# Kernel optimization log

Hardware: AMD Instinct MI355X
Metric: run time of the kernel (lower is better)

The kernel has to match this reference:

```python
import jax, jax.numpy as jnp
import numpy as np

L, H, N = 4096, 256, 64  # seq_len, hidden_size, hippo_n
EPS = 1e-5


def setup_inputs() -> dict:
    key = jax.random.key(0)
    ks = jax.random.split(key, 8)
    x = jax.random.normal(ks[0], (L, H), jnp.float32)
    # S4D-Lin style initialization for the diagonal SSM (H independent SSMs of state size N)
    Lambda_re = -0.5 * jnp.ones((H, N), jnp.float32)
    Lambda_im = jnp.tile(jnp.pi * jnp.arange(N, dtype=jnp.float32), (H, 1))
    B_re = jnp.ones((H, N), jnp.float32)
    B_im = jnp.zeros((H, N), jnp.float32)
    C_re = jax.random.normal(ks[1], (H, N), jnp.float32) * (0.5 ** 0.5)
    C_im = jax.random.normal(ks[2], (H, N), jnp.float32) * (0.5 ** 0.5)
    D = jax.random.normal(ks[3], (H,), jnp.float32)
    log_step = jax.random.uniform(ks[4], (H,), jnp.float32,
                                  minval=jnp.log(0.001), maxval=jnp.log(0.1))
    ln_w = jnp.ones((H,), jnp.float32)
    ln_b = jnp.zeros((H,), jnp.float32)
    sc = 1.0 / jnp.sqrt(jnp.float32(H))
    W1 = jax.random.normal(ks[5], (H, H), jnp.float32) * sc
    b1 = jnp.zeros((H,), jnp.float32)
    W2 = jax.random.normal(ks[6], (H, H), jnp.float32) * sc
    b2 = jnp.zeros((H,), jnp.float32)
    return {"x": x, "Lambda_re": Lambda_re, "Lambda_im": Lambda_im,
            "B_re": B_re, "B_im": B_im, "C_re": C_re, "C_im": C_im,
            "D": D, "log_step": log_step, "ln_w": ln_w, "ln_b": ln_b,
            "W1": W1, "b1": b1, "W2": W2, "b2": b2}


def reference(x, Lambda_re, Lambda_im, B_re, B_im, C_re, C_im, D, log_step,
              ln_w, ln_b, W1, b1, W2, b2):
    skip = x
    # per-token LayerNorm over the H feature axis (eqx.nn.LayerNorm, eps=1e-5)
    mu = jnp.mean(x, axis=-1, keepdims=True)
    var = jnp.mean(jnp.square(x - mu), axis=-1, keepdims=True)
    xn = (x - mu) / jnp.sqrt(var + EPS) * ln_w + ln_b  # [L, H]

    # ZOH discretization of the diagonal SSM (the cell.ssm(L) step)
    Lam = Lambda_re + 1j * Lambda_im                     # [H, N] complex64
    dt = jnp.exp(log_step)[:, None]                      # [H, 1]
    Ab = jnp.exp(Lam * dt)                               # [H, N]
    Bb = (Ab - 1.0) / Lam * (B_re + 1j * B_im)           # [H, N]
    C = C_re + 1j * C_im                                 # [H, N]

    def step(s, u):  # s: [H, N] complex state, u: [H] input at one time step
        s = Ab * s + Bb * u[:, None]
        y = 2.0 * jnp.einsum('hn,hn->h', C, s).real + D * u
        return s, y

    s0 = jnp.zeros((H, N), jnp.complex64)
    hidden, ys = jax.lax.scan(step, s0, xn)              # ys: [L, H]

    g = jax.nn.gelu(ys)
    out = (g @ W1.T + b1) * jax.nn.sigmoid(g @ W2.T + b2)  # GLU epilogue
    return (hidden, skip + out)
```

## Files before the change

### kernel.cpp

```cpp
#include <hip/hip_runtime.h>
#include <hip/hip_bf16.h>

#define LSEQ 4096
#define HDIM 256
#define NS   64
#define PC   32
#define MC   128

typedef __attribute__((ext_vector_type(8))) short short8;
typedef __attribute__((ext_vector_type(4))) float floatx4;

__device__ __forceinline__ short b16(float x) {
    __hip_bfloat16 h = __float2bfloat16(x);
    return *(reinterpret_cast<short*>(&h));
}
__device__ __forceinline__ float bf2f(unsigned short u) {
    unsigned int v = ((unsigned int)u) << 16;
    return __uint_as_float(v);
}
__device__ __forceinline__ unsigned int pk2(float a, float b) {
    return (unsigned int)(unsigned short)b16(a) | ((unsigned int)(unsigned short)b16(b) << 16);
}
__device__ __forceinline__ void cmul(float& xr, float& xi, float yr, float yi) {
    float r = xr * yr - xi * yi;
    float i = xr * yi + xi * yr;
    xr = r; xi = i;
}

__global__ __launch_bounds__(256) void k_pre(const float* __restrict__ x,
                                             const float* __restrict__ lnw,
                                             const float* __restrict__ lnb,
                                             const float* __restrict__ W1,
                                             const float* __restrict__ W2,
                                             float* __restrict__ xnT,
                                             unsigned short* __restrict__ w1b,
                                             unsigned short* __restrict__ w2b) {
    int t = threadIdx.x;
    if (blockIdx.x >= 256) {
        int g = (blockIdx.x - 256) * 256 + t;
        float4 a = ((const float4*)W1)[g];
        float4 c = ((const float4*)W2)[g];
        ushort4 o1, o2;
        o1.x = (unsigned short)b16(a.x); o1.y = (unsigned short)b16(a.y);
        o1.z = (unsigned short)b16(a.z); o1.w = (unsigned short)b16(a.w);
        o2.x = (unsigned short)b16(c.x); o2.y = (unsigned short)b16(c.y);
        o2.z = (unsigned short)b16(c.z); o2.w = (unsigned short)b16(c.w);
        ((ushort4*)w1b)[g] = o1;
        ((ushort4*)w2b)[g] = o2;
        return;
    }
    __shared__ float tile[16][257];
    __shared__ float smu[16], srs[16];
    int l0 = blockIdx.x * 16;
#pragma unroll
    for (int i = 0; i < 16; ++i)
        tile[i][t] = x[(size_t)(l0 + i) * HDIM + t];
    __syncthreads();
    int wv = t >> 6, lane = t & 63;
#pragma unroll
    for (int k = 0; k < 4; ++k) {
        int i = wv * 4 + k;
        float s = 0.f, s2 = 0.f;
#pragma unroll
        for (int q = 0; q < 4; ++q) {
            float v = tile[i][lane + 64 * q];
            s += v; s2 += v * v;
        }
#pragma unroll
        for (int o = 32; o; o >>= 1) {
            s  += __shfl_xor(s, o);
            s2 += __shfl_xor(s2, o);
        }
        if (lane == 0) {
            float m = s * (1.0f / HDIM);
            smu[i] = m;
            srs[i] = rsqrtf(s2 * (1.0f / HDIM) - m * m + 1e-5f);
        }
    }
    __syncthreads();
    float wh = lnw[t], bh = lnb[t];
    float o[16];
#pragma unroll
    for (int i = 0; i < 16; ++i)
        o[i] = (tile[i][t] - smu[i]) * srs[i] * wh + bh;
    float4* dst = (float4*)(xnT + (size_t)t * LSEQ + l0);
#pragma unroll
    for (int k = 0; k < 4; ++k)
        dst[k] = make_float4(o[4 * k], o[4 * k + 1], o[4 * k + 2], o[4 * k + 3]);
}

__device__ __forceinline__ void ssm_consts(const float* Lre, const float* Lim,
                                           const float* Bre, const float* Bim,
                                           float dt, int idx,
                                           float& are, float& aim, float& bre, float& bim) {
    float lre = Lre[idx], lim = Lim[idx];
    float er = expf(lre * dt);
    float sa, ca;
    sincosf(lim * dt, &sa, &ca);
    are = er * ca; aim = er * sa;
    float inv = 1.0f / (lre * lre + lim * lim);
    float nre = are - 1.0f, nim = aim;
    float tre = (nre * lre + nim * lim) * inv;
    float tim = (nim * lre - nre * lim) * inv;
    float br = Bre[idx], bi = Bim[idx];
    bre = tre * br - tim * bi;
    bim = tre * bi + tim * br;
}

__global__ __launch_bounds__(512) void k_scan(const float* __restrict__ xnT,
                                              const float* __restrict__ Lre,
                                              const float* __restrict__ Lim,
                                              const float* __restrict__ Bre,
                                              const float* __restrict__ Bim,
                                              const float* __restrict__ Cre,
                                              const float* __restrict__ Cim,
                                              const float* __restrict__ Dv,
                                              const float* __restrict__ lstep,
                                              __hip_bfloat16* __restrict__ gb,
                                              float* __restrict__ hid,
                                              int interleaved) {
    __shared__ __align__(16) unsigned char ldsb[60672];
    short* ubf = (short*)(ldsb);
    short* Xm  = (short*)(ldsb + 8704);
    float* Ff  = (float*)(ldsb + 43520);
    short* S0s = (short*)(ldsb + 43520);
    float* Kt  = (float*)(ldsb + 60160);

    int h = blockIdx.x >> 1, half = blockIdx.x & 1;
    int tid = threadIdx.x;
    int wv = __builtin_amdgcn_readfirstlane(tid) >> 6;
    int lane = tid & 63;
    int l15 = lane & 15, q = lane >> 4;
    const float* uh = xnT + (size_t)h * LSEQ;

    float dt = expf(lstep[h]);
    float Dh = Dv[h];

    float are, aim, bre, bim;
    ssm_consts(Lre, Lim, Bre, Bim, dt, h * NS + lane, are, aim, bre, bim);
    float cre = Cre[h * NS + lane], cim = Cim[h * NS + lane];

    float A2r = are, A2i = aim;   cmul(A2r, A2i, are, aim);
    float A4r = A2r, A4i = A2i;   cmul(A4r, A4i, A2r, A2i);
    float A8r = A4r, A8i = A4i;   cmul(A8r, A8i, A4r, A4i);
    float A16r = A8r, A16i = A8i;  cmul(A16r, A16i, A8r, A8i);
    float A32r = A16r, A32i = A16i; cmul(A32r, A32i, A16r, A16i);
    float A64r = A32r, A64i = A32i; cmul(A64r, A64i, A32r, A32i);

    {
        int i8 = tid * 8;
        float4 v0 = *(const float4*)(uh + i8);
        float4 v1 = *(const float4*)(uh + i8 + 4);
        int c = i8 >> 7, col = i8 & 127;
        unsigned int* d = (unsigned int*)(ubf + c * 136 + col);
        d[0] = pk2(v0.x, v0.y);
        d[1] = pk2(v0.z, v0.w);
        d[2] = pk2(v1.x, v1.y);
        d[3] = pk2(v1.z, v1.w);
    }

    {
        float cbre = cre * bre - cim * bim;
        float cbim = cre * bim + cim * bre;
        float pr = 1.f, pi = 0.f;
        if (wv & 1) cmul(pr, pi, A16r, A16i);
        if (wv & 2) cmul(pr, pi, A32r, A32i);
        if (wv & 4) cmul(pr, pi, A64r, A64i);
#pragma unroll
        for (int i = 0; i < 16; ++i) {
            float kj = 2.f * (cbre * pr - cbim * pi);
#pragma unroll
            for (int o = 1; o <= 32; o <<= 1) kj += __shfl_xor(kj, o);
            if (lane == 0) Kt[16 * wv + i] = kj;
            cmul(pr, pi, are, aim);
        }
    }

    {
        int v = 7 - wv;
        float pr = 1.f, pi = 0.f;
        if (v & 1) cmul(pr, pi, A16r, A16i);
        if (v & 2) cmul(pr, pi, A32r, A32i);
        if (v & 4) cmul(pr, pi, A64r, A64i);
        short8 rrB, riB, rrA, riA;
#pragma unroll
        for (int e = 7; e >= 0; --e) {
            rrB[e] = b16(bre * pr - bim * pi);
            riB[e] = b16(bre * pi + bim * pr);
            cmul(pr, pi, are, aim);
        }
#pragma unroll
        for (int e = 7; e >= 0; --e) {
            rrA[e] = b16(bre * pr - bim * pi);
            riA[e] = b16(bre * pi + bim * pr);
            if (e) cmul(pr, pi, are, aim);
        }
        *(short8*)(Xm + lane * 136 + 16 * wv) = rrA;
        *(short8*)(Xm + lane * 136 + 16 * wv + 8) = rrB;
        *(short8*)(Xm + (64 + lane) * 136 + 16 * wv) = riA;
        *(short8*)(Xm + (64 + lane) * 136 + 16 * wv + 8) = riB;
    }
    __syncthreads();

    {
        floatx4 fa[2];
        fa[0] = (floatx4){0.f, 0.f, 0.f, 0.f};
        fa[1] = (floatx4){0.f, 0.f, 0.f, 0.f};
#pragma unroll
        for (int ks = 0; ks < 4; ++ks) {
            short8 am = *(short8*)(Xm + (16 * wv + l15) * 136 + 32 * ks + 8 * q);
#pragma unroll
            for (int ct = 0; ct < 2; ++ct) {
                short8 bu = *(short8*)(ubf + (16 * ct + l15) * 136 + 32 * ks + 8 * q);
                fa[ct] = __builtin_amdgcn_mfma_f32_16x16x32_bf16(am, bu, fa[ct], 0, 0, 0);
            }
        }
#pragma unroll
        for (int ct = 0; ct < 2; ++ct) {
            int c = 16 * ct + l15;
            float* fp = Ff + c * 130;
            int s = 16 * wv + 4 * q;
#pragma unroll
            for (int reg = 0; reg < 4; ++reg) {
                fp[(wv < 4) ? (s + reg) : (1 + s + reg)] = fa[ct][reg];
            }
        }
    }
    __syncthreads();

    if (wv == 0) {
        float a128r = A64r, a128i = A64i;
        cmul(a128r, a128i, A64r, A64i);
        float sre = 0.f, sim = 0.f;
        for (int c = 0; c < PC; ++c) {
            float fre = Ff[c * 130 + lane];
            float fim = Ff[c * 130 + 65 + lane];
            ((unsigned int*)(ldsb + 43520 + 272 * c))[lane] = pk2(sre, sim);
            float nr = fmaf(a128r, sre, fmaf(-a128i, sim, fre));
            float ni = fmaf(a128r, sim, fmaf( a128i, sre, fim));
            sre = nr; sim = ni;
        }
        if (half == 1) {
            if (interleaved) {
                ((float2*)hid)[h * NS + lane] = make_float2(sre, sim);
            } else {
                hid[h * NS + lane] = sre;
            }
        }
    } else {
        float A7r = A4r, A7i = A4i;
        cmul(A7r, A7i, A2r, A2i);
        cmul(A7r, A7i, are, aim);
        float pr = 1.f, pi = 0.f;
        if (wv & 1) cmul(pr, pi, are, aim);
        if (wv & 2) cmul(pr, pi, A2r, A2i);
        if (wv & 4) cmul(pr, pi, A4r, A4i);
#pragma unroll
        for (int i = 0; i < 19; ++i) {
            int t = (wv - 1) + 7 * i;
            if (t < 128) {
                float er =  2.f * (cre * pr - cim * pi);
                float en = -2.f * (cre * pi + cim * pr);
                ((unsigned int*)(ldsb + 8704 + 272 * t))[lane] = pk2(er, en);
            }
            cmul(pr, pi, A7r, A7i);
        }
    }

    floatx4 Y = (floatx4){0.f, 0.f, 0.f, 0.f};
    {
        int row = 16 * wv + l15;
#pragma unroll
        for (int ks = 0; ks < 4; ++ks) {
            short8 ta;
#pragma unroll
            for (int e = 0; e < 8; ++e) {
                int col = 32 * ks + 8 * q + e;
                float kv = Kt[(row - col) & 127];
                ta[e] = (col <= row) ? b16(kv) : (short)0;
            }
            short8 bu = *(short8*)(ubf + (16 * half + l15) * 136 + 32 * ks + 8 * q);
            Y = __builtin_amdgcn_mfma_f32_16x16x32_bf16(ta, bu, Y, 0, 0, 0);
        }
    }
    __syncthreads();

#pragma unroll
    for (int ks = 0; ks < 4; ++ks) {
        short8 ea = *(short8*)(Xm + (16 * wv + l15) * 136 + 32 * ks + 8 * q);
        short8 sf = *(short8*)(S0s + (16 * half + l15) * 136 + 32 * ks + 8 * q);
        Y = __builtin_amdgcn_mfma_f32_16x16x32_bf16(ea, sf, Y, 0, 0, 0);
    }

    {
        int c = 16 * half + l15;
#pragma unroll
        for (int reg = 0; reg < 4; ++reg) {
            int t = 16 * wv + 4 * q + reg;
            int l = c * MC + t;
            float u = bf2f((unsigned short)ubf[c * 136 + t]);
            float y = Y[reg] + Dh * u;
            float z = 0.7978845608028654f * fmaf(0.044715f, y * y * y, y);
            float e = __expf(2.f * z);
            float th = 1.f - 2.f / (e + 1.f);
            float gg = 0.5f * y * (1.f + th);
            gb[((size_t)l << 8) + h] = __float2bfloat16(gg);
        }
    }
}

__global__ __launch_bounds__(64) void k_glu_mfma(const unsigned short* __restrict__ gbs,
                                                 const unsigned short* __restrict__ w1b,
                                                 const unsigned short* __restrict__ w2b,
                                                 const float* __restrict__ b1v,
                                                 const float* __restrict__ b2v,
                                                 const float* __restrict__ x,
                                                 float* __restrict__ out) {
    int bx = blockIdx.x;
    int m0 = (bx >> 4) * 32;
    int n0 = (bx & 15) * 16;
    int lane = threadIdx.x;
    int t = lane & 15, q = lane >> 4;

    floatx4 acc[2][2];
    acc[0][0] = (floatx4){0,0,0,0}; acc[0][1] = (floatx4){0,0,0,0};
    acc[1][0] = (floatx4){0,0,0,0}; acc[1][1] = (floatx4){0,0,0,0};

    const unsigned short* A0 = gbs + (size_t)(m0 + t) * HDIM + q * 8;
    const unsigned short* A1 = A0 + 16 * HDIM;
    const unsigned short* B1 = w1b + (size_t)(n0 + t) * HDIM + q * 8;
    const unsigned short* B2 = w2b + (size_t)(n0 + t) * HDIM + q * 8;

#pragma unroll
    for (int ks = 0; ks < 8; ++ks) {
        int off = ks * 32;
        short8 a0 = *(const short8*)(A0 + off);
        short8 a1 = *(const short8*)(A1 + off);
        short8 b1 = *(const short8*)(B1 + off);
        short8 b2 = *(const short8*)(B2 + off);
        acc[0][0] = __builtin_amdgcn_mfma_f32_16x16x32_bf16(a0, b1, acc[0][0], 0, 0, 0);
        acc[1][0] = __builtin_amdgcn_mfma_f32_16x16x32_bf16(a1, b1, acc[1][0], 0, 0, 0);
        acc[0][1] = __builtin_amdgcn_mfma_f32_16x16x32_bf16(a0, b2, acc[0][1], 0, 0, 0);
        acc[1][1] = __builtin_amdgcn_mfma_f32_16x16x32_bf16(a1, b2, acc[1][1], 0, 0, 0);
    }

    int hh = n0 + t;
    float bb1 = b1v[hh], bb2 = b2v[hh];
#pragma unroll
    for (int mt = 0; mt < 2; ++mt) {
#pragma unroll
        for (int reg = 0; reg < 4; ++reg) {
            int l = m0 + mt * 16 + q * 4 + reg;
            float a  = acc[mt][0][reg] + bb1;
            float sg = 1.f / (1.f + __expf(-(acc[mt][1][reg] + bb2)));
            out[(size_t)l * HDIM + hh] = fmaf(a, sg, x[(size_t)l * HDIM + hh]);
        }
    }
}

extern "C" void kernel_launch(void* const* d_in, const int* in_sizes, int n_in,
                              void* d_out, int out_size, void* d_ws, size_t ws_size,
                              hipStream_t stream) {
    (void)in_sizes; (void)n_in; (void)ws_size;
    const float* x     = (const float*)d_in[0];
    const float* Lre   = (const float*)d_in[1];
    const float* Lim   = (const float*)d_in[2];
    const float* Bre   = (const float*)d_in[3];
    const float* Bim   = (const float*)d_in[4];
    const float* Cre   = (const float*)d_in[5];
    const float* Cim   = (const float*)d_in[6];
    const float* Dv    = (const float*)d_in[7];
    const float* lstep = (const float*)d_in[8];
    const float* lnw   = (const float*)d_in[9];
    const float* lnb   = (const float*)d_in[10];
    const float* W1    = (const float*)d_in[11];
    const float* b1    = (const float*)d_in[12];
    const float* W2    = (const float*)d_in[13];
    const float* b2    = (const float*)d_in[14];

    float* ws   = (float*)d_ws;
    float* xnT  = ws;
    unsigned short* gb  = (unsigned short*)(xnT + (size_t)HDIM * LSEQ);
    unsigned short* w1b = gb + (size_t)LSEQ * HDIM;
    unsigned short* w2b = w1b + HDIM * HDIM;

    int interleaved = (out_size == LSEQ * HDIM + 2 * HDIM * NS) ? 1 : 0;
    float* hid  = (float*)d_out;
    float* outp = (float*)d_out + (interleaved ? 2 * HDIM * NS : HDIM * NS);

    k_pre      <<<256 + 64, 256, 0, stream>>>(x, lnw, lnb, W1, W2, xnT, w1b, w2b);
    k_scan     <<<2 * HDIM, 512, 0, stream>>>(xnT, Lre, Lim, Bre, Bim, Cre, Cim,
                                              Dv, lstep, (__hip_bfloat16*)gb, hid, interleaved);
    k_glu_mfma <<<128 * 16, 64, 0, stream>>>(gb, w1b, w2b, b1, b2, x, outp);
}
```

Measured before the change: 115.6 us.

## Convert GLU weights to bf16 inside GEMM and replace scan kernel shuffle reductions

Removes the separate bf16 conversion of W1/W2 from the prologue kernel. The GLU MFMA kernel now loads the fp32 weights and converts them in registers, which drops the workspace writes but makes every GEMM block read twice the weight bytes and redo the conversion. In the scan kernel, the per-row 6-step butterfly shuffle reductions of the convolution kernel coefficients are replaced by writing partials to LDS and summing them with vectorized reads plus two shuffles. This adds an extra barrier and reuses the Xm LDS region.

```diff
diff --git a/kernel.cpp b/kernel.cpp
--- a/kernel.cpp
+++ b/kernel.cpp
@@ -30,25 +30,8 @@
 __global__ __launch_bounds__(256) void k_pre(const float* __restrict__ x,
                                              const float* __restrict__ lnw,
                                              const float* __restrict__ lnb,
-                                             const float* __restrict__ W1,
-                                             const float* __restrict__ W2,
-                                             float* __restrict__ xnT,
-                                             unsigned short* __restrict__ w1b,
-                                             unsigned short* __restrict__ w2b) {
+                                             float* __restrict__ xnT) {
     int t = threadIdx.x;
-    if (blockIdx.x >= 256) {
-        int g = (blockIdx.x - 256) * 256 + t;
-        float4 a = ((const float4*)W1)[g];
-        float4 c = ((const float4*)W2)[g];
-        ushort4 o1, o2;
-        o1.x = (unsigned short)b16(a.x); o1.y = (unsigned short)b16(a.y);
-        o1.z = (unsigned short)b16(a.z); o1.w = (unsigned short)b16(a.w);
-        o2.x = (unsigned short)b16(c.x); o2.y = (unsigned short)b16(c.y);
-        o2.z = (unsigned short)b16(c.z); o2.w = (unsigned short)b16(c.w);
-        ((ushort4*)w1b)[g] = o1;
-        ((ushort4*)w2b)[g] = o2;
-        return;
-    }
     __shared__ float tile[16][257];
     __shared__ float smu[16], srs[16];
     int l0 = blockIdx.x * 16;
@@ -122,6 +105,7 @@
     __shared__ __align__(16) unsigned char ldsb[60672];
     short* ubf = (short*)(ldsb);
     short* Xm  = (short*)(ldsb + 8704);
+    float* Kc  = (float*)(ldsb + 8704);
     float* Ff  = (float*)(ldsb + 43520);
     short* S0s = (short*)(ldsb + 43520);
     float* Kt  = (float*)(ldsb + 60160);
@@ -168,13 +152,21 @@
         if (wv & 4) cmul(pr, pi, A64r, A64i);
 #pragma unroll
         for (int i = 0; i < 16; ++i) {
-            float kj = 2.f * (cbre * pr - cbim * pi);
-#pragma unroll
-            for (int o = 1; o <= 32; o <<= 1) kj += __shfl_xor(kj, o);
-            if (lane == 0) Kt[16 * wv + i] = kj;
+            Kc[(16 * wv + i) * 68 + lane] = 2.f * (cbre * pr - cbim * pi);
             cmul(pr, pi, are, aim);
         }
     }
+    {
+        int r = 16 * wv + l15;
+        const float4* rp = (const float4*)(Kc + r * 68 + 16 * q);
+        float4 v0 = rp[0], v1 = rp[1], v2 = rp[2], v3 = rp[3];
+        float s = ((v0.x + v0.y) + (v0.z + v0.w)) + ((v1.x + v1.y) + (v1.z + v1.w))
+                + ((v2.x + v2.y) + (v2.z + v2.w)) + ((v3.x + v3.y) + (v3.z + v3.w));
+        s += __shfl_xor(s, 16);
+        s += __shfl_xor(s, 32);
+        if (q == 0) Kt[r] = s;
+    }
+    __syncthreads();
 
     {
         int v = 7 - wv;
@@ -310,8 +302,8 @@
 }
 
 __global__ __launch_bounds__(64) void k_glu_mfma(const unsigned short* __restrict__ gbs,
-                                                 const unsigned short* __restrict__ w1b,
-                                                 const unsigned short* __restrict__ w2b,
+                                                 const float* __restrict__ W1,
+                                                 const float* __restrict__ W2,
                                                  const float* __restrict__ b1v,
                                                  const float* __restrict__ b2v,
                                                  const float* __restrict__ x,
@@ -328,16 +320,24 @@
 
     const unsigned short* A0 = gbs + (size_t)(m0 + t) * HDIM + q * 8;
     const unsigned short* A1 = A0 + 16 * HDIM;
-    const unsigned short* B1 = w1b + (size_t)(n0 + t) * HDIM + q * 8;
-    const unsigned short* B2 = w2b + (size_t)(n0 + t) * HDIM + q * 8;
+    const float* W1r = W1 + (size_t)(n0 + t) * HDIM;
+    const float* W2r = W2 + (size_t)(n0 + t) * HDIM;
 
 #pragma unroll
     for (int ks = 0; ks < 8; ++ks) {
         int off = ks * 32;
         short8 a0 = *(const short8*)(A0 + off);
         short8 a1 = *(const short8*)(A1 + off);
-        short8 b1 = *(const short8*)(B1 + off);
-        short8 b2 = *(const short8*)(B2 + off);
+        int woff = off + q * 8;
+        float4 wa0 = *(const float4*)(W1r + woff);
+        float4 wa1 = *(const float4*)(W1r + woff + 4);
+        float4 wb0 = *(const float4*)(W2r + woff);
+        float4 wb1 = *(const float4*)(W2r + woff + 4);
+        short8 b1, b2;
+        b1[0] = b16(wa0.x); b1[1] = b16(wa0.y); b1[2] = b16(wa0.z); b1[3] = b16(wa0.w);
+        b1[4] = b16(wa1.x); b1[5] = b16(wa1.y); b1[6] = b16(wa1.z); b1[7] = b16(wa1.w);
+        b2[0] = b16(wb0.x); b2[1] = b16(wb0.y); b2[2] = b16(wb0.z); b2[3] = b16(wb0.w);
+        b2[4] = b16(wb1.x); b2[5] = b16(wb1.y); b2[6] = b16(wb1.z); b2[7] = b16(wb1.w);
         acc[0][0] = __builtin_amdgcn_mfma_f32_16x16x32_bf16(a0, b1, acc[0][0], 0, 0, 0);
         acc[1][0] = __builtin_amdgcn_mfma_f32_16x16x32_bf16(a1, b1, acc[1][0], 0, 0, 0);
         acc[0][1] = __builtin_amdgcn_mfma_f32_16x16x32_bf16(a0, b2, acc[0][1], 0, 0, 0);
@@ -381,15 +381,13 @@
     float* ws   = (float*)d_ws;
     float* xnT  = ws;
     unsigned short* gb  = (unsigned short*)(xnT + (size_t)HDIM * LSEQ);
-    unsigned short* w1b = gb + (size_t)LSEQ * HDIM;
-    unsigned short* w2b = w1b + HDIM * HDIM;
 
     int interleaved = (out_size == LSEQ * HDIM + 2 * HDIM * NS) ? 1 : 0;
     float* hid  = (float*)d_out;
     float* outp = (float*)d_out + (interleaved ? 2 * HDIM * NS : HDIM * NS);
 
-    k_pre      <<<256 + 64, 256, 0, stream>>>(x, lnw, lnb, W1, W2, xnT, w1b, w2b);
+    k_pre      <<<256, 256, 0, stream>>>(x, lnw, lnb, xnT);
     k_scan     <<<2 * HDIM, 512, 0, stream>>>(xnT, Lre, Lim, Bre, Bim, Cre, Cim,
                                               Dv, lstep, (__hip_bfloat16*)gb, hid, interleaved);
-    k_glu_mfma <<<128 * 16, 64, 0, stream>>>(gb, w1b, w2b, b1, b2, x, outp);
-}
+    k_glu_mfma <<<128 * 16, 64, 0, stream>>>(gb, W1, W2, b1, b2, x, outp);
+}
```

Result: no change. 117.6 us (+1.8%).
